# Performance work log

Measured on AMD Instinct MI355X. Metric: run time of the kernel, lower is better.

Reference implementation:

```python
import jax, jax.numpy as jnp
import numpy as np

B, C, H, W = 8, 384, 32, 32
N = 4                      # d_state
DI = 2 * C                 # d_inner = ssm_ratio * dim
R = -(-C // 16)            # dt_rank = ceil(dim/16) = 24
K = 4                      # scan directions
HID = 4 * C                # mlp hidden


def layer_norm(x, g, b, eps=1e-5):
    mu = jnp.mean(x, -1, keepdims=True)
    var = jnp.mean((x - mu) ** 2, -1, keepdims=True)
    return (x - mu) * jax.lax.rsqrt(var + eps) * g + b


def setup_inputs() -> dict:
    key = jax.random.key(0)
    ks = jax.random.split(key, 20)
    s = lambda k, shape, sc=0.02: jax.random.normal(k, shape, jnp.float32) * sc
    inp = {
        "x": jax.random.normal(ks[0], (B, C, H, W), jnp.float32),
        "ln1_g": jnp.ones((C,), jnp.float32), "ln1_b": jnp.zeros((C,), jnp.float32),
        "in_proj_W": s(ks[1], (2 * DI, C)),
        "conv_W": s(ks[2], (DI, 1, 3, 3), 0.1), "conv_b": jnp.zeros((DI,), jnp.float32),
        "x_proj_W": s(ks[3], (K, R + 2 * N, DI)),
        "dt_W": s(ks[4], (K, DI, R), 0.1), "dt_b": s(ks[5], (K, DI), 0.1),
        "A_log": jnp.log(jnp.tile(jnp.arange(1, N + 1, dtype=jnp.float32), (K, DI, 1))),
        "Ds": jnp.ones((K, DI), jnp.float32),
        "out_norm_g": jnp.ones((DI,), jnp.float32), "out_norm_b": jnp.zeros((DI,), jnp.float32),
        "out_proj_W": s(ks[6], (C, DI)),
        "ln2_g": jnp.ones((C,), jnp.float32), "ln2_b": jnp.zeros((C,), jnp.float32),
        "fc1_W": s(ks[7], (HID, C)), "fc1_b": jnp.zeros((HID,), jnp.float32),
        "fc2_W": s(ks[8], (C, HID)), "fc2_b": jnp.zeros((C,), jnp.float32),
    }
    return inp


def _block(x, ln1_g, ln1_b, in_proj_W, conv_W, conv_b, x_proj_W, dt_W, dt_b,
           A_log, Ds, out_norm_g, out_norm_b, out_proj_W, ln2_g, ln2_b,
           fc1_W, fc1_b, fc2_W, fc2_b):
    # x: (B,C,H,W) -> channels-last (B,H,W,C) as in mamba_fusion4
    xin = jnp.transpose(x, (0, 2, 3, 1))
    L = H * W
    shortcut = xin
    xn = layer_norm(xin, ln1_g, ln1_b)
    # ---- SS2D ----
    xz = jnp.einsum('bhwc,ec->bhwe', xn, in_proj_W)           # (B,H,W,2*DI)
    xs_, z = jnp.split(xz, 2, axis=-1)
    xc = jnp.transpose(xs_, (0, 3, 1, 2))                     # (B,DI,H,W)
    xc = jax.lax.conv_general_dilated(xc, conv_W, (1, 1), ((1, 1), (1, 1)),
                                      feature_group_count=DI)
    xc = jax.nn.silu(xc + conv_b[None, :, None, None])
    # cross-scan: 4 directions
    x_hw = xc.reshape(B, DI, L)
    x_wh = jnp.transpose(xc, (0, 1, 3, 2)).reshape(B, DI, L)
    xs = jnp.stack([x_hw, x_wh, jnp.flip(x_hw, -1), jnp.flip(x_wh, -1)], axis=1)  # (B,K,DI,L)
    x_dbl = jnp.einsum('bkdl,kcd->bkcl', xs, x_proj_W)
    dts, Bs, Cs = x_dbl[:, :, :R], x_dbl[:, :, R:R + N], x_dbl[:, :, R + N:]
    dts = jnp.einsum('bkrl,kdr->bkdl', dts, dt_W)
    dt = jax.nn.softplus(dts + dt_b[None, :, :, None])        # (B,K,DI,L)
    A = -jnp.exp(A_log)                                       # (K,DI,N)
    # selective scan, L-leading
    dt_l = jnp.transpose(dt, (3, 0, 1, 2))
    xs_l = jnp.transpose(xs, (3, 0, 1, 2))
    Bs_l = jnp.transpose(Bs, (3, 0, 1, 2))
    Cs_l = jnp.transpose(Cs, (3, 0, 1, 2))

    def step(h, inp):
        dtt, xt, Bt, Ct = inp                                  # (B,K,DI),(B,K,DI),(B,K,N),(B,K,N)
        h = jnp.exp(dtt[..., None] * A) * h + (dtt * xt)[..., None] * Bt[:, :, None, :]
        yt = jnp.einsum('bkdn,bkn->bkd', h, Ct)
        return h, yt

    h0 = jnp.zeros((B, K, DI, N), xs.dtype)
    _, ys = jax.lax.scan(step, h0, (dt_l, xs_l, Bs_l, Cs_l))   # ys: (L,B,K,DI)
    ys = jnp.transpose(ys, (1, 2, 3, 0))                       # (B,K,DI,L)
    ys = ys + xs * Ds[None, :, :, None]                        # skip D*u per direction
    # merge directions (invert flips / transposes)
    inv = jnp.flip(ys[:, 2:4], -1)
    wh = lambda t: jnp.transpose(t.reshape(B, DI, W, H), (0, 1, 3, 2)).reshape(B, DI, L)
    y = ys[:, 0] + inv[:, 0] + wh(ys[:, 1]) + wh(inv[:, 1])    # (B,DI,L)
    y = jnp.transpose(y, (0, 2, 1)).reshape(B, H, W, DI)
    y = layer_norm(y, out_norm_g, out_norm_b)
    y = y * jax.nn.silu(z)
    y = jnp.einsum('bhwd,cd->bhwc', y, out_proj_W)
    xr = shortcut + y
    # ---- MLP ----
    m = layer_norm(xr, ln2_g, ln2_b)
    m = jax.nn.gelu(jnp.einsum('bhwc,ec->bhwe', m, fc1_W) + fc1_b)
    m = jnp.einsum('bhwe,ce->bhwc', m, fc2_W) + fc2_b
    return xr + m                                              # (B,H,W,C)


def reference(x, ln1_g, ln1_b, in_proj_W, conv_W, conv_b, x_proj_W, dt_W, dt_b,
              A_log, Ds, out_norm_g, out_norm_b, out_proj_W, ln2_g, ln2_b,
              fc1_W, fc1_b, fc2_W, fc2_b):
    return _block(x, ln1_g, ln1_b, in_proj_W, conv_W, conv_b, x_proj_W, dt_W, dt_b,
                  A_log, Ds, out_norm_g, out_norm_b, out_proj_W, ln2_g, ln2_b,
                  fc1_W, fc1_b, fc2_W, fc2_b)
```

## Files before the change

### kernel.cpp

```cpp
#include <hip/hip_runtime.h>
#include <hip/hip_bf16.h>
#include <math.h>

#define LQ 1024
#define CC 384
#define DI 768
#define RR 24
#define NN 4
#define BB 8
#define NC 32
#define CL 32
#define LDP 40

typedef __attribute__((ext_vector_type(8))) short bf16x8;
typedef __attribute__((ext_vector_type(4))) float f32x4;

__device__ __forceinline__ float siluf(float v) { return v / (1.f + __expf(-v)); }
__device__ __forceinline__ float softplus_fast(float v) {
  float av = fabsf(v);
  float e = __expf(-av);
  return fmaxf(v, 0.f) + 0.69314718f * __log2f(1.f + e);
}
__device__ __forceinline__ float geluf(float x) {
  float u = 0.7978845608028654f * (x + 0.044715f * x * x * x);
  float e = __expf(2.f * u);
  float t = 1.f - 2.f / (e + 1.f);
  return 0.5f * x * (1.f + t);
}
__device__ __forceinline__ int trp(int l) { return ((l & 31) << 5) | (l >> 5); }
__device__ __forceinline__ short f2bf(float f) {
  union { float f; unsigned u; } v; v.f = f;
  unsigned r = (v.u + 0x7fffu + ((v.u >> 16) & 1u)) >> 16;
  return (short)r;
}
__device__ __forceinline__ float bf2f(unsigned short u) {
  union { unsigned u; float f; } v; v.u = ((unsigned)u) << 16; return v.f;
}
__device__ __forceinline__ bf16x8 pack8(float4 u, float4 v) {
  bf16x8 r;
  r[0] = f2bf(u.x); r[1] = f2bf(u.y); r[2] = f2bf(u.z); r[3] = f2bf(u.w);
  r[4] = f2bf(v.x); r[5] = f2bf(v.y); r[6] = f2bf(v.z); r[7] = f2bf(v.w);
  return r;
}
__device__ __forceinline__ void gload_lds16(const void* g, void* l) {
  __builtin_amdgcn_global_load_lds(
      (const __attribute__((address_space(1))) void*)g,
      (__attribute__((address_space(3))) void*)l, 16, 0, 0);
}
__device__ __forceinline__ void tile_barrier() {
  asm volatile("s_waitcnt lgkmcnt(0)" ::: "memory");
  __builtin_amdgcn_s_barrier();
  __builtin_amdgcn_sched_barrier(0);
}

__global__ __launch_bounds__(256) void wcvt_kernel(
    const float* __restrict__ w0, const float* __restrict__ w1,
    const float* __restrict__ w2, const float* __restrict__ w3,
    unsigned short* __restrict__ dst) {
  int gid = blockIdx.x * 256 + threadIdx.x;
  int e = gid * 8;
  const float* src; int off;
  if (e < 589824)        { src = w0; off = e; }
  else if (e < 884736)   { src = w1; off = e - 589824; }
  else if (e < 1474560)  { src = w2; off = e - 884736; }
  else                   { src = w3; off = e - 1474560; }
  float4 a = *(const float4*)(src + off);
  float4 b = *(const float4*)(src + off + 4);
  *(bf16x8*)(dst + e) = pack8(a, b);
}

__global__ __launch_bounds__(256) void ln1_transpose(
    const float* __restrict__ x, const float* __restrict__ g, const float* __restrict__ b,
    unsigned short* __restrict__ xn, unsigned short* __restrict__ xT) {
  __shared__ float xt[CC][65];
  __shared__ float reds[4][64], redq[4][64];
  __shared__ float mus[64], rvs[64];
  int blk = blockIdx.x;
  int bb = blk >> 4, l0 = (blk & 15) * 64;
  int tid = threadIdx.x;
  const float* xb = x + (size_t)bb * CC * LQ + l0;
#pragma unroll
  for (int it = 0; it < 96; ++it) {
// ... 207 lines not shown
  };
  auto storeT = [&](short* Ad, short* Wd, const uint4& pa, const float4* pw) {
    *(uint4*)&Ad[ar * LDP + ac] = pa;
    short* wdst = &Wd[wr * LDP + wc];
#pragma unroll
    for (int i = 0; i < WL / 2; ++i)
      *(bf16x8*)(wdst + i * 8) = pack8(pw[2 * i], pw[2 * i + 1]);
  };
  auto computeT = [&](const short* Ab, const short* Wb) {
    bf16x8 af[2], bf[NF];
#pragma unroll
    for (int i = 0; i < 2; ++i)
      af[i] = *(const bf16x8*)&Ab[(wm + i * 16 + l15) * LDP + l4 * 8];
#pragma unroll
    for (int j = 0; j < NF; ++j)
      bf[j] = *(const bf16x8*)&Wb[(wn + j * 16 + l15) * LDP + l4 * 8];
#pragma unroll
    for (int i = 0; i < 2; ++i)
#pragma unroll
      for (int j = 0; j < NF; ++j)
        acc[i][j] = __builtin_amdgcn_mfma_f32_16x16x32_bf16(af[i], bf[j], acc[i][j], 0, 0, 0);
  };

  const int NT = K >> 5;
  loadT(0, pa0, pw0);
  storeT(As0, Ws0, pa0, pw0);
  loadT(1, pa1, pw1);
  tile_barrier();
  for (int t = 0; t < NT; t += 2) {
    if (t + 2 < NT) loadT(t + 2, pa0, pw0);
    computeT(As0, Ws0);
    storeT(As1, Ws1, pa1, pw1);
    tile_barrier();
    if (t + 3 < NT) loadT(t + 3, pa1, pw1);
    computeT(As1, Ws1);
    if (t + 2 < NT) storeT(As0, Ws0, pa0, pw0);
    tile_barrier();
  }
#pragma unroll
  for (int i = 0; i < 2; ++i) {
    int mb = bm + wm + i * 16 + l4 * 4;
#pragma unroll
    for (int j = 0; j < NF; ++j) {
      int n = bn + wn + j * 16 + l15;
#pragma unroll
      for (int q = 0; q < 4; ++q) {
        int m = mb + q;
        ((float*)out0)[(size_t)m * N + n] = acc[i][j][q];
      }
    }
  }
}

__global__ __launch_bounds__(256) void dt_gemm(
    const float* __restrict__ xdbl, const float* __restrict__ dtW,
    const float* __restrict__ dtb, unsigned short* __restrict__ dt_all) {
  __shared__ short smem[128 * 136];
  short* As = smem;
  short* Ws = smem + 128 * LDP;
  const int tid = threadIdx.x;
  const int bm = blockIdx.x * 128;
  const int kk = blockIdx.y / 6, nt = blockIdx.y % 6;
  const int n0 = nt * 128;
  const int lane = tid & 63, w = tid >> 6;
  const int wm = (w >> 1) * 64, wn = (w & 1) * 64;
  const int l15 = lane & 15, l4 = lane >> 4;
  const int r = tid >> 1, half = (tid & 1) * 16;
  {
    const float* Ag = xdbl + (size_t)(bm + r) * 128 + kk * 32 + half;
    float4 a0 = *(const float4*)(Ag);
    float4 a1 = *(const float4*)(Ag + 4);
    float4 a2 = *(const float4*)(Ag + 8);
    float4 a3 = *(const float4*)(Ag + 12);
    short* asw = &As[r * LDP + half];
    *(bf16x8*)asw = pack8(a0, a1);
    *(bf16x8*)(asw + 8) = pack8(a2, a3);
    const float* Wg = dtW + ((size_t)kk * DI + n0 + r) * RR;
    bf16x8 qa, qb;
    if (half == 0) {
      float4 w0 = *(const float4*)(Wg);
      float4 w1 = *(const float4*)(Wg + 4);
      float4 w2 = *(const float4*)(Wg + 8);
      float4 w3 = *(const float4*)(Wg + 12);
      qa = pack8(w0, w1);
      qb = pack8(w2, w3);
    } else {
      float4 w0 = *(const float4*)(Wg + 16);
      float4 w1 = *(const float4*)(Wg + 20);
      qa = pack8(w0, w1);
      qb[0] = 0; qb[1] = 0; qb[2] = 0; qb[3] = 0;
      qb[4] = 0; qb[5] = 0; qb[6] = 0; qb[7] = 0;
    }
    short* wsw = &Ws[r * LDP + half];
    *(bf16x8*)wsw = qa;
    *(bf16x8*)(wsw + 8) = qb;
  }
  __syncthreads();
  f32x4 acc[4][4] = {};
  {
    const short* ap = &As[(wm + l15) * LDP + l4 * 8];
    const short* bp = &Ws[(wn + l15) * LDP + l4 * 8];
    bf16x8 af[4], bf[4];
#pragma unroll
    for (int f = 0; f < 4; ++f) af[f] = *(const bf16x8*)(ap + f * 16 * LDP);
#pragma unroll
    for (int f = 0; f < 4; ++f) bf[f] = *(const bf16x8*)(bp + f * 16 * LDP);
#pragma unroll
    for (int i = 0; i < 4; ++i)
#pragma unroll
      for (int j = 0; j < 4; ++j)
        acc[i][j] = __builtin_amdgcn_mfma_f32_16x16x32_bf16(af[i], bf[j], acc[i][j], 0, 0, 0);
  }
  __syncthreads();
#pragma unroll
  for (int j = 0; j < 4; ++j) {
    int col = wn + j * 16 + l15;
    float bv = dtb[kk * DI + n0 + col];
#pragma unroll
    for (int i = 0; i < 4; ++i) {
      int mrow = wm + i * 16 + l4 * 4;
#pragma unroll
      for (int q = 0; q < 4; ++q)
        smem[(mrow + q) * 136 + col] = f2bf(softplus_fast(acc[i][j][q] + bv));
    }
  }
  __syncthreads();
  const int row0 = tid >> 4, cg = (tid & 15) * 8;
#pragma unroll
  for (int it = 0; it < 8; ++it) {
    int row = row0 + it * 16;
    bf16x8 v = *(const bf16x8*)&smem[row * 136 + cg];
    *(bf16x8*)&dt_all[(size_t)(bm + row) * 3072 + kk * DI + n0 + cg] = v;
  }
}

__global__ __launch_bounds__(256) void conv_silu_kernel(
    const unsigned short* __restrict__ xs_, const float* __restrict__ cw,
    const float* __restrict__ cb, unsigned short* __restrict__ xcT) {
  int idx = blockIdx.x * 256 + threadIdx.x;
  int dg = idx % 96;
  int rem = idx / 96;
  int hq = rem & 7;
  int w = (rem >> 3) & 31;
  int b = rem >> 8;
  int d0 = dg * 8;
  int h0 = hq * 4;
  float wbuf[72];
#pragma unroll
  for (int i = 0; i < 18; ++i)
    *(float4*)&wbuf[i * 4] = *(const float4*)(cw + d0 * 9 + i * 4);
  float bias[8];
  *(float4*)&bias[0] = *(const float4*)(cb + d0);
  *(float4*)&bias[4] = *(const float4*)(cb + d0 + 4);
  float acc[4][8];
#pragma unroll
  for (int i = 0; i < 4; ++i)
#pragma unroll
    for (int j = 0; j < 8; ++j) acc[i][j] = bias[j];
  const unsigned short* xb = xs_ + (size_t)b * LQ * DI + d0;
#pragma unroll
  for (int hh = -1; hh <= 4; ++hh) {
    int h = h0 + hh;
    if (h < 0 || h > 31) continue;
#pragma unroll
    for (int dw = -1; dw <= 1; ++dw) {
      int ww = w + dw;
      if (ww < 0 || ww > 31) continue;
      bf16x8 xv = *(const bf16x8*)&xb[(size_t)(h * 32 + ww) * DI];
      float xf[8];
#pragma unroll
      for (int j = 0; j < 8; ++j) xf[j] = bf2f((unsigned short)xv[j]);
#pragma unroll
      for (int i = 0; i < 4; ++i) {
        int dh = hh - i;
        if (dh < -1 || dh > 1) continue;
        int tap = (dh + 1) * 3 + (dw + 1);
#pragma unroll
        for (int j = 0; j < 8; ++j) acc[i][j] += xf[j] * wbuf[j * 9 + tap];
      }
    }
  }
  unsigned short* ob = xcT + (size_t)b * LQ * DI + d0;
#pragma unroll
  for (int i = 0; i < 4; ++i) {
    bf16x8 v;
#pragma unroll
    for (int j = 0; j < 8; ++j) v[j] = f2bf(siluf(acc[i][j]));
    *(bf16x8*)&ob[(size_t)((h0 + i) * 32 + w) * DI] = v;
  }
}

__global__ __launch_bounds__(256) void scan_pass1(
    const unsigned short* __restrict__ xcT, const float* __restrict__ xdbl,
    const unsigned short* __restrict__ dtq,
    const float* __restrict__ A_log, float* __restrict__ Hc, float* __restrict__ Pc) {
  int c = blockIdx.x, dc = blockIdx.y, bk = blockIdx.z;
  int b = bk >> 2, k = bk & 3;
  int d = dc * 256 + threadIdx.x;
  float4 al = *(const float4*)&A_log[((size_t)k * DI + d) * NN];
  float A[NN] = {-__expf(al.x), -__expf(al.y), -__expf(al.z), -__expf(al.w)};
  float h[NN] = {0.f, 0.f, 0.f, 0.f}, P[NN] = {1.f, 1.f, 1.f, 1.f};
  const int kg = k & 1;
  const bool fl = k >= 2;
  int pos0 = kg ? c : c * CL;
  int dpos = kg ? 32 : 1;
  if (fl) { pos0 = 1023 - pos0; dpos = -dpos; }
  const unsigned short* dtp = dtq + ((size_t)b * LQ + pos0) * 3072 + k * DI + d;
  const unsigned short* xcp = xcT + ((size_t)b * LQ + pos0) * DI + d;
  const float* xdp = xdbl + ((size_t)b * LQ + pos0) * 128 + k * 32 + 24;
  const ptrdiff_t sDT = (ptrdiff_t)dpos * 3072;
  const ptrdiff_t sXC = (ptrdiff_t)dpos * DI;
  const ptrdiff_t sXD = (ptrdiff_t)dpos * 128;
  for (int j = 0; j < CL; ++j) {
    float dt = bf2f(*dtp);
    float xv = bf2f(*xcp);
    float4 Bv = *(const float4*)xdp;
    float dx = dt * xv;
    float a;
    a = __expf(dt * A[0]); h[0] = a * h[0] + dx * Bv.x; P[0] *= a;
    a = __expf(dt * A[1]); h[1] = a * h[1] + dx * Bv.y; P[1] *= a;
    a = __expf(dt * A[2]); h[2] = a * h[2] + dx * Bv.z; P[2] *= a;
    a = __expf(dt * A[3]); h[3] = a * h[3] + dx * Bv.w; P[3] *= a;
    dtp += sDT; xcp += sXC; xdp += sXD;
  }
  size_t base = (((size_t)bk * NC + c) * DI + d) * 4;
  *(float4*)&Hc[base] = make_float4(h[0], h[1], h[2], h[3]);
  *(float4*)&Pc[base] = make_float4(P[0], P[1], P[2], P[3]);
}

__global__ __launch_bounds__(256) void scan_pass2(
    float* __restrict__ Hc, const float* __restrict__ Pc) {
  int idx = blockIdx.x * 256 + threadIdx.x;
  int bk = idx / DI, d = idx - bk * DI;
  float4 hin = make_float4(0.f, 0.f, 0.f, 0.f);
  for (int c = 0; c < NC; ++c) {
    size_t base = (((size_t)bk * NC + c) * DI + d) * 4;
    float4 hl = *(const float4*)&Hc[base];
    float4 p = *(const float4*)&Pc[base];
    *(float4*)&Hc[base] = hin;
    hin.x = hl.x + p.x * hin.x;
    hin.y = hl.y + p.y * hin.y;
    hin.z = hl.z + p.z * hin.z;
    hin.w = hl.w + p.w * hin.w;
  }
}

__global__ __launch_bounds__(256) void scan_pass3(
    const unsigned short* __restrict__ xcT, const float* __restrict__ xdbl,
    const unsigned short* __restrict__ dtq,
    const float* __restrict__ A_log, const float* __restrict__ Ds,
    const float* __restrict__ Hin,
    unsigned short* __restrict__ ym1, unsigned short* __restrict__ ym2) {
  __shared__ unsigned short ylds[CL][256];
  int c = blockIdx.x, dc = blockIdx.y, bg = blockIdx.z;
  int b = bg >> 1, g = bg & 1;
  int tid = threadIdx.x;
  int d = dc * 256 + tid;
  int ka = g, kb = g + 2;
  int ca = c, cb = NC - 1 - c;
  float4 ala = *(const float4*)&A_log[((size_t)ka * DI + d) * NN];
  float4 alb = *(const float4*)&A_log[((size_t)kb * DI + d) * NN];
  float Aa[NN] = {-__expf(ala.x), -__expf(ala.y), -__expf(ala.z), -__expf(ala.w)};
  float Ab[NN] = {-__expf(alb.x), -__expf(alb.y), -__expf(alb.z), -__expf(alb.w)};
  float Da = Ds[ka * DI + d], Db = Ds[kb * DI + d];
  size_t basea = (((size_t)(b * 4 + ka) * NC + ca) * DI + d) * 4;
  size_t baseb = (((size_t)(b * 4 + kb) * NC + cb) * DI + d) * 4;
  float4 h4a = *(const float4*)&Hin[basea];
  float4 h4b = *(const float4*)&Hin[baseb];
  float ha[NN] = {h4a.x, h4a.y, h4a.z, h4a.w};
  float hb[NN] = {h4b.x, h4b.y, h4b.z, h4b.w};
  unsigned short* ym = g ? ym2 : ym1;
  int pa0 = g ? ca : ca * CL;
  int dpa = g ? 32 : 1;
  int pb0 = g ? (1023 - cb) : (1023 - cb * CL);
  const unsigned short* dta_p = dtq + ((size_t)b * LQ + pa0) * 3072 + ka * DI + d;
  const unsigned short* dtb_p = dtq + ((size_t)b * LQ + pb0) * 3072 + kb * DI + d;
  const unsigned short* xca_p = xcT + ((size_t)b * LQ + pa0) * DI + d;
  const unsigned short* xcb_p = xcT + ((size_t)b * LQ + pb0) * DI + d;
  const float* xda_p = xdbl + ((size_t)b * LQ + pa0) * 128 + ka * 32 + 24;
  const float* xdb_p = xdbl + ((size_t)b * LQ + pb0) * 128 + kb * 32 + 24;
  const ptrdiff_t sDT = (ptrdiff_t)dpa * 3072;
  const ptrdiff_t sXC = (ptrdiff_t)dpa * DI;
  const ptrdiff_t sXD = (ptrdiff_t)dpa * 128;
  for (int j = 0; j < CL; ++j) {
    float dta = bf2f(*dta_p);
    float dtb2 = bf2f(*dtb_p);
    float xa = bf2f(*xca_p);
    float xb = bf2f(*xcb_p);
    float4 Ba = *(const float4*)xda_p;
    float4 Ca = *(const float4*)(xda_p + 4);
    float4 Bb = *(const float4*)xdb_p;
    float4 Cb = *(const float4*)(xdb_p + 4);
    float dxa = dta * xa, dxb = dtb2 * xb;
    float ya = xa * Da, yb = xb * Db;
    float a;
    a = __expf(dta * Aa[0]); ha[0] = a * ha[0] + dxa * Ba.x; ya += ha[0] * Ca.x;
    a = __expf(dta * Aa[1]); ha[1] = a * ha[1] + dxa * Ba.y; ya += ha[1] * Ca.y;
    a = __expf(dta * Aa[2]); ha[2] = a * ha[2] + dxa * Ba.z; ya += ha[2] * Ca.z;
    a = __expf(dta * Aa[3]); ha[3] = a * ha[3] + dxa * Ba.w; ya += ha[3] * Ca.w;
    a = __expf(dtb2 * Ab[0]); hb[0] = a * hb[0] + dxb * Bb.x; yb += hb[0] * Cb.x;
    a = __expf(dtb2 * Ab[1]); hb[1] = a * hb[1] + dxb * Bb.y; yb += hb[1] * Cb.y;
    a = __expf(dtb2 * Ab[2]); hb[2] = a * hb[2] + dxb * Bb.z; yb += hb[2] * Cb.z;
    a = __expf(dtb2 * Ab[3]); hb[3] = a * hb[3] + dxb * Bb.w; yb += hb[3] * Cb.w;
    if (j < CL / 2) {
      ylds[j][tid] = (unsigned short)f2bf(ya);
      ylds[CL - 1 - j][tid] = (unsigned short)f2bf(yb);
    } else {
      ylds[j][tid] = (unsigned short)f2bf(bf2f(ylds[j][tid]) + ya);
      ylds[CL - 1 - j][tid] = (unsigned short)f2bf(bf2f(ylds[CL - 1 - j][tid]) + yb);
    }
    dta_p += sDT; dtb_p -= sDT;
    xca_p += sXC; xcb_p -= sXC;
    xda_p += sXD; xdb_p -= sXD;
  }
  unsigned short* ymp = ym + ((size_t)b * LQ + pa0) * DI + d;
  for (int s = 0; s < CL; ++s) {
    *ymp = ylds[s][tid];
    ymp += sXC;
  }
}

__global__ __launch_bounds__(256) void outnorm_mult_kernel(
    const unsigned short* __restrict__ ym1, const unsigned short* __restrict__ ym2,
    const unsigned short* __restrict__ z, const float* __restrict__ g,
    const float* __restrict__ bta, unsigned short* __restrict__ out) {
  int t = blockIdx.x, tid = threadIdx.x;
  __shared__ float red[8];
  float v[3]; float s = 0.f, sq = 0.f;
#pragma unroll
  for (int i = 0; i < 3; ++i) {
    int dd = tid + i * 256;
    float y = bf2f(ym1[(size_t)t * DI + dd]) + bf2f(ym2[(size_t)t * DI + dd]);
    v[i] = y; s += y; sq += y * y;
  }
#pragma unroll
  for (int off = 32; off > 0; off >>= 1) { s += __shfl_xor(s, off); sq += __shfl_xor(sq, off); }
  int wid = tid >> 6;
  if ((tid & 63) == 0) { red[wid] = s; red[4 + wid] = sq; }
  __syncthreads();
  s = red[0] + red[1] + red[2] + red[3];
  sq = red[4] + red[5] + red[6] + red[7];
  float mu = s * (1.f / DI), var = sq * (1.f / DI) - mu * mu;
  float r = rsqrtf(var + 1e-5f);
#pragma unroll
  for (int i = 0; i < 3; ++i) {
    int dd = tid + i * 256;
    float zv = bf2f(z[(size_t)t * DI + dd]);
    out[(size_t)t * DI + dd] =
        (unsigned short)f2bf(((v[i] - mu) * r * g[dd] + bta[dd]) * siluf(zv));
  }
}

extern "C" void kernel_launch(void* const* d_in, const int* in_sizes, int n_in,
                              void* d_out, int out_size, void* d_ws, size_t ws_size,
                              hipStream_t stream) {
  const float* x          = (const float*)d_in[0];
  const float* ln1_g      = (const float*)d_in[1];
  const float* ln1_b      = (const float*)d_in[2];
  const float* in_proj_W  = (const float*)d_in[3];
  const float* conv_W     = (const float*)d_in[4];
  const float* conv_b     = (const float*)d_in[5];
  const float* x_proj_W   = (const float*)d_in[6];
  const float* dt_W       = (const float*)d_in[7];
  const float* dt_b       = (const float*)d_in[8];
  const float* A_log      = (const float*)d_in[9];
  const float* Ds         = (const float*)d_in[10];
  const float* out_norm_g = (const float*)d_in[11];
  const float* out_norm_b = (const float*)d_in[12];
  const float* out_proj_W = (const float*)d_in[13];
  const float* ln2_g      = (const float*)d_in[14];
  const float* ln2_b      = (const float*)d_in[15];
  const float* fc1_W      = (const float*)d_in[16];
  const float* fc1_b      = (const float*)d_in[17];
  const float* fc2_W      = (const float*)d_in[18];
  const float* fc2_b      = (const float*)d_in[19];

  const int M = BB * LQ;
  char* RA = (char*)d_ws;
  char* RB = RA + 12582912;
  char* RC = RB + 25165824;
  char* RD = RC + 12582912;
  char* RE = RD + 25165824;
  char* RF = RE + 12582912;
  char* RG = RF + 4194304;
  char* RH = RG + 50331648;

  unsigned short* xn  = (unsigned short*)RA;
  float*          Hc  = (float*)RA;
  float*          xr  = (float*)RA;
  unsigned short* xs_ = (unsigned short*)RB;
  float*          Pc  = (float*)RB;
  unsigned short* ym1 = (unsigned short*)RB;
  unsigned short* m1  = (unsigned short*)RB;
  unsigned short* z   = (unsigned short*)RC;
  unsigned short* m0  = (unsigned short*)RC;
  unsigned short* ym2 = (unsigned short*)RD;
  unsigned short* xcT = (unsigned short*)RE;
  unsigned short* mn  = (unsigned short*)RE;
  float*          xdbl = (float*)RF;
  unsigned short* dtq = (unsigned short*)RG;
  unsigned short* xT  = (unsigned short*)RH;
  unsigned short* wbf = (unsigned short*)(RH + 6291456);
  unsigned short* wb_inproj  = wbf;
  unsigned short* wb_outproj = wbf + 589824;
  unsigned short* wb_fc1     = wbf + 884736;
  unsigned short* wb_fc2     = wbf + 1474560;

  wcvt_kernel<<<1008, 256, 0, stream>>>(in_proj_W, out_proj_W, fc1_W, fc2_W, wbf);
  ln1_transpose<<<128, 256, 0, stream>>>(x, ln1_g, ln1_b, xn, xT);
  gemm_lds<0, 128><<<dim3(M / 128, 12), 256, 0, stream>>>(
      xn, wb_inproj, xs_, z, nullptr, nullptr, M, 1536, CC);
  conv_silu_kernel<<<768, 256, 0, stream>>>(xs_, conv_W, conv_b, xcT);
  gemm_mfma<4, 64><<<dim3(M / 64, 2), 256, 0, stream>>>(
      xcT, x_proj_W, xdbl, nullptr, nullptr, nullptr, M, 128, DI);
  dt_gemm<<<dim3(M / 128, 24), 256, 0, stream>>>(xdbl, dt_W, dt_b, dtq);
  scan_pass1<<<dim3(NC, 3, BB * 4), 256, 0, stream>>>(
      xcT, xdbl, dtq, A_log, Hc, Pc);
  scan_pass2<<<(BB * 4 * DI) / 256, 256, 0, stream>>>(Hc, Pc);
  scan_pass3<<<dim3(NC, 3, BB * 2), 256, 0, stream>>>(
      xcT, xdbl, dtq, A_log, Ds, Hc, ym1, ym2);
  outnorm_mult_kernel<<<M, 256, 0, stream>>>(ym1, ym2, z, out_norm_g, out_norm_b, mn);
  gemm_lds<1, 64><<<dim3(M / 64, 3), 256, 0, stream>>>(
      mn, wb_outproj, xr, nullptr, nullptr, xT, M, 384, DI);
  ln2_kernel<<<M, 64, 0, stream>>>(xr, ln2_g, ln2_b, m0);
  gemm_lds<2, 128><<<dim3(M / 128, 12), 256, 0, stream>>>(
      m0, wb_fc1, m1, nullptr, fc1_b, nullptr, M, 1536, CC);
  gemm_lds<3, 64><<<dim3(M / 64, 3), 256, 0, stream>>>(
      m1, wb_fc2, (float*)d_out, nullptr, fc2_b, xr, M, 384, 1536);
}
```

Baseline: 227.7 us.

## Fuse dt projection and softplus into scan passes, drop dt_gemm

New measurement: 282.6 us. +24.1%, slower.

```diff
diff --git a/kernel.cpp b/kernel.cpp
--- a/kernel.cpp
+++ b/kernel.cpp
@@ -341,88 +341,6 @@
   }
 }
 
-__global__ __launch_bounds__(256) void dt_gemm(
-    const float* __restrict__ xdbl, const float* __restrict__ dtW,
-    const float* __restrict__ dtb, unsigned short* __restrict__ dt_all) {
-  __shared__ short smem[128 * 136];
-  short* As = smem;
-  short* Ws = smem + 128 * LDP;
-  const int tid = threadIdx.x;
-  const int bm = blockIdx.x * 128;
-  const int kk = blockIdx.y / 6, nt = blockIdx.y % 6;
-  const int n0 = nt * 128;
-  const int lane = tid & 63, w = tid >> 6;
-  const int wm = (w >> 1) * 64, wn = (w & 1) * 64;
-  const int l15 = lane & 15, l4 = lane >> 4;
-  const int r = tid >> 1, half = (tid & 1) * 16;
-  {
-    const float* Ag = xdbl + (size_t)(bm + r) * 128 + kk * 32 + half;
-    float4 a0 = *(const float4*)(Ag);
-    float4 a1 = *(const float4*)(Ag + 4);
-    float4 a2 = *(const float4*)(Ag + 8);
-    float4 a3 = *(const float4*)(Ag + 12);
-    short* asw = &As[r * LDP + half];
-    *(bf16x8*)asw = pack8(a0, a1);
-    *(bf16x8*)(asw + 8) = pack8(a2, a3);
-    const float* Wg = dtW + ((size_t)kk * DI + n0 + r) * RR;
-    bf16x8 qa, qb;
-    if (half == 0) {
-      float4 w0 = *(const float4*)(Wg);
-      float4 w1 = *(const float4*)(Wg + 4);
-      float4 w2 = *(const float4*)(Wg + 8);
-      float4 w3 = *(const float4*)(Wg + 12);
-      qa = pack8(w0, w1);
-      qb = pack8(w2, w3);
-    } else {
-      float4 w0 = *(const float4*)(Wg + 16);
-      float4 w1 = *(const float4*)(Wg + 20);
-      qa = pack8(w0, w1);
-      qb[0] = 0; qb[1] = 0; qb[2] = 0; qb[3] = 0;
-      qb[4] = 0; qb[5] = 0; qb[6] = 0; qb[7] = 0;
-    }
-    short* wsw = &Ws[r * LDP + half];
-    *(bf16x8*)wsw = qa;
-    *(bf16x8*)(wsw + 8) = qb;
-  }
-  __syncthreads();
-  f32x4 acc[4][4] = {};
-  {
-    const short* ap = &As[(wm + l15) * LDP + l4 * 8];
-    const short* bp = &Ws[(wn + l15) * LDP + l4 * 8];
-    bf16x8 af[4], bf[4];
-#pragma unroll
-    for (int f = 0; f < 4; ++f) af[f] = *(const bf16x8*)(ap + f * 16 * LDP);
-#pragma unroll
-    for (int f = 0; f < 4; ++f) bf[f] = *(const bf16x8*)(bp + f * 16 * LDP);
-#pragma unroll
-    for (int i = 0; i < 4; ++i)
-#pragma unroll
-      for (int j = 0; j < 4; ++j)
-        acc[i][j] = __builtin_amdgcn_mfma_f32_16x16x32_bf16(af[i], bf[j], acc[i][j], 0, 0, 0);
-  }
-  __syncthreads();
-#pragma unroll
-  for (int j = 0; j < 4; ++j) {
-    int col = wn + j * 16 + l15;
-    float bv = dtb[kk * DI + n0 + col];
-#pragma unroll
-    for (int i = 0; i < 4; ++i) {
-      int mrow = wm + i * 16 + l4 * 4;
-#pragma unroll
-      for (int q = 0; q < 4; ++q)
-        smem[(mrow + q) * 136 + col] = f2bf(softplus_fast(acc[i][j][q] + bv));
-    }
-  }
-  __syncthreads();
-  const int row0 = tid >> 4, cg = (tid & 15) * 8;
-#pragma unroll
-  for (int it = 0; it < 8; ++it) {
-    int row = row0 + it * 16;
-    bf16x8 v = *(const bf16x8*)&smem[row * 136 + cg];
-    *(bf16x8*)&dt_all[(size_t)(bm + row) * 3072 + kk * DI + n0 + cg] = v;
-  }
-}
-
 __global__ __launch_bounds__(256) void conv_silu_kernel(
     const unsigned short* __restrict__ xs_, const float* __restrict__ cw,
     const float* __restrict__ cb, unsigned short* __restrict__ xcT) {
@@ -481,36 +399,51 @@
 
 __global__ __launch_bounds__(256) void scan_pass1(
     const unsigned short* __restrict__ xcT, const float* __restrict__ xdbl,
-    const unsigned short* __restrict__ dtq,
+    const float* __restrict__ dtW, const float* __restrict__ dtb,
     const float* __restrict__ A_log, float* __restrict__ Hc, float* __restrict__ Pc) {
+  __shared__ float xl[CL][36];
   int c = blockIdx.x, dc = blockIdx.y, bk = blockIdx.z;
   int b = bk >> 2, k = bk & 3;
-  int d = dc * 256 + threadIdx.x;
-  float4 al = *(const float4*)&A_log[((size_t)k * DI + d) * NN];
-  float A[NN] = {-__expf(al.x), -__expf(al.y), -__expf(al.z), -__expf(al.w)};
-  float h[NN] = {0.f, 0.f, 0.f, 0.f}, P[NN] = {1.f, 1.f, 1.f, 1.f};
+  int tid = threadIdx.x;
+  int d = dc * 256 + tid;
   const int kg = k & 1;
   const bool fl = k >= 2;
   int pos0 = kg ? c : c * CL;
   int dpos = kg ? 32 : 1;
   if (fl) { pos0 = 1023 - pos0; dpos = -dpos; }
-  const unsigned short* dtp = dtq + ((size_t)b * LQ + pos0) * 3072 + k * DI + d;
+  {
+    int j = tid >> 3, q = tid & 7;
+    int pos = pos0 + j * dpos;
+    *(float4*)&xl[j][q * 4] =
+        *(const float4*)(xdbl + ((size_t)b * LQ + pos) * 128 + k * 32 + q * 4);
+  }
+  float4 al = *(const float4*)&A_log[((size_t)k * DI + d) * NN];
+  float A[NN] = {-__expf(al.x), -__expf(al.y), -__expf(al.z), -__expf(al.w)};
+  float w[RR];
+  const float* wp = dtW + ((size_t)k * DI + d) * RR;
+#pragma unroll
+  for (int r = 0; r < RR; r += 4) {
+    float4 t4 = *(const float4*)(wp + r);
+    w[r] = t4.x; w[r + 1] = t4.y; w[r + 2] = t4.z; w[r + 3] = t4.w;
+  }
+  float dbias = dtb[k * DI + d];
+  float h[NN] = {0.f, 0.f, 0.f, 0.f}, P[NN] = {1.f, 1.f, 1.f, 1.f};
   const unsigned short* xcp = xcT + ((size_t)b * LQ + pos0) * DI + d;
-  const float* xdp = xdbl + ((size_t)b * LQ + pos0) * 128 + k * 32 + 24;
-  const ptrdiff_t sDT = (ptrdiff_t)dpos * 3072;
   const ptrdiff_t sXC = (ptrdiff_t)dpos * DI;
-  const ptrdiff_t sXD = (ptrdiff_t)dpos * 128;
+  __syncthreads();
   for (int j = 0; j < CL; ++j) {
-    float dt = bf2f(*dtp);
+    float dtr = dbias;
+#pragma unroll
+    for (int r = 0; r < RR; ++r) dtr += xl[j][r] * w[r];
+    float dt = softplus_fast(dtr);
     float xv = bf2f(*xcp);
-    float4 Bv = *(const float4*)xdp;
     float dx = dt * xv;
     float a;
-    a = __expf(dt * A[0]); h[0] = a * h[0] + dx * Bv.x; P[0] *= a;
-    a = __expf(dt * A[1]); h[1] = a * h[1] + dx * Bv.y; P[1] *= a;
-    a = __expf(dt * A[2]); h[2] = a * h[2] + dx * Bv.z; P[2] *= a;
-    a = __expf(dt * A[3]); h[3] = a * h[3] + dx * Bv.w; P[3] *= a;
-    dtp += sDT; xcp += sXC; xdp += sXD;
+    a = __expf(dt * A[0]); h[0] = a * h[0] + dx * xl[j][24]; P[0] *= a;
+    a = __expf(dt * A[1]); h[1] = a * h[1] + dx * xl[j][25]; P[1] *= a;
+    a = __expf(dt * A[2]); h[2] = a * h[2] + dx * xl[j][26]; P[2] *= a;
+    a = __expf(dt * A[3]); h[3] = a * h[3] + dx * xl[j][27]; P[3] *= a;
+    xcp += sXC;
   }
   size_t base = (((size_t)bk * NC + c) * DI + d) * 4;
   *(float4*)&Hc[base] = make_float4(h[0], h[1], h[2], h[3]);
@@ -536,22 +469,46 @@
 
 __global__ __launch_bounds__(256) void scan_pass3(
     const unsigned short* __restrict__ xcT, const float* __restrict__ xdbl,
-    const unsigned short* __restrict__ dtq,
+    const float* __restrict__ dtW, const float* __restrict__ dtb,
     const float* __restrict__ A_log, const float* __restrict__ Ds,
     const float* __restrict__ Hin,
     unsigned short* __restrict__ ym1, unsigned short* __restrict__ ym2) {
   __shared__ unsigned short ylds[CL][256];
+  __shared__ float xla[CL][36], xlb[CL][36];
   int c = blockIdx.x, dc = blockIdx.y, bg = blockIdx.z;
   int b = bg >> 1, g = bg & 1;
   int tid = threadIdx.x;
   int d = dc * 256 + tid;
   int ka = g, kb = g + 2;
   int ca = c, cb = NC - 1 - c;
+  int pa0 = g ? ca : ca * CL;
+  int dpa = g ? 32 : 1;
+  int pb0 = g ? (1023 - cb) : (1023 - cb * CL);
+  {
+    int j = tid >> 3, q = tid & 7;
+    int posa = pa0 + j * dpa;
+    int posb = pb0 - j * dpa;
+    *(float4*)&xla[j][q * 4] =
+        *(const float4*)(xdbl + ((size_t)b * LQ + posa) * 128 + ka * 32 + q * 4);
+    *(float4*)&xlb[j][q * 4] =
+        *(const float4*)(xdbl + ((size_t)b * LQ + posb) * 128 + kb * 32 + q * 4);
+  }
   float4 ala = *(const float4*)&A_log[((size_t)ka * DI + d) * NN];
   float4 alb = *(const float4*)&A_log[((size_t)kb * DI + d) * NN];
   float Aa[NN] = {-__expf(ala.x), -__expf(ala.y), -__expf(ala.z), -__expf(ala.w)};
   float Ab[NN] = {-__expf(alb.x), -__expf(alb.y), -__expf(alb.z), -__expf(alb.w)};
   float Da = Ds[ka * DI + d], Db = Ds[kb * DI + d];
+  float wa[RR], wb[RR];
+  const float* wap = dtW + ((size_t)ka * DI + d) * RR;
+  const float* wbp = dtW + ((size_t)kb * DI + d) * RR;
+#pragma unroll
+  for (int r = 0; r < RR; r += 4) {
+    float4 t4 = *(const float4*)(wap + r);
+    wa[r] = t4.x; wa[r + 1] = t4.y; wa[r + 2] = t4.z; wa[r + 3] = t4.w;
+    float4 u4 = *(const float4*)(wbp + r);
+    wb[r] = u4.x; wb[r + 1] = u4.y; wb[r + 2] = u4.z; wb[r + 3] = u4.w;
+  }
+  float biasa = dtb[ka * DI + d], biasb = dtb[kb * DI + d];
   size_t basea = (((size_t)(b * 4 + ka) * NC + ca) * DI + d) * 4;
   size_t baseb = (((size_t)(b * 4 + kb) * NC + cb) * DI + d) * 4;
   float4 h4a = *(const float4*)&Hin[basea];
@@ -559,38 +516,32 @@
   float ha[NN] = {h4a.x, h4a.y, h4a.z, h4a.w};
   float hb[NN] = {h4b.x, h4b.y, h4b.z, h4b.w};
   unsigned short* ym = g ? ym2 : ym1;
-  int pa0 = g ? ca : ca * CL;
-  int dpa = g ? 32 : 1;
-  int pb0 = g ? (1023 - cb) : (1023 - cb * CL);
-  const unsigned short* dta_p = dtq + ((size_t)b * LQ + pa0) * 3072 + ka * DI + d;
-  const unsigned short* dtb_p = dtq + ((size_t)b * LQ + pb0) * 3072 + kb * DI + d;
   const unsigned short* xca_p = xcT + ((size_t)b * LQ + pa0) * DI + d;
   const unsigned short* xcb_p = xcT + ((size_t)b * LQ + pb0) * DI + d;
-  const float* xda_p = xdbl + ((size_t)b * LQ + pa0) * 128 + ka * 32 + 24;
-  const float* xdb_p = xdbl + ((size_t)b * LQ + pb0) * 128 + kb * 32 + 24;
-  const ptrdiff_t sDT = (ptrdiff_t)dpa * 3072;
   const ptrdiff_t sXC = (ptrdiff_t)dpa * DI;
-  const ptrdiff_t sXD = (ptrdiff_t)dpa * 128;
+  __syncthreads();
   for (int j = 0; j < CL; ++j) {
-    float dta = bf2f(*dta_p);
-    float dtb2 = bf2f(*dtb_p);
+    float dtra = biasa, dtrb = biasb;
+#pragma unroll
+    for (int r = 0; r < RR; ++r) {
+      dtra += xla[j][r] * wa[r];
+      dtrb += xlb[j][r] * wb[r];
+    }
+    float dta = softplus_fast(dtra);
+    float dtb2 = softplus_fast(dtrb);
     float xa = bf2f(*xca_p);
     float xb = bf2f(*xcb_p);
-    float4 Ba = *(const float4*)xda_p;
-    float4 Ca = *(const float4*)(xda_p + 4);
-    float4 Bb = *(const float4*)xdb_p;
-    float4 Cb = *(const float4*)(xdb_p + 4);
     float dxa = dta * xa, dxb = dtb2 * xb;
     float ya = xa * Da, yb = xb * Db;
     float a;
-    a = __expf(dta * Aa[0]); ha[0] = a * ha[0] + dxa * Ba.x; ya += ha[0] * Ca.x;
-    a = __expf(dta * Aa[1]); ha[1] = a * ha[1] + dxa * Ba.y; ya += ha[1] * Ca.y;
-    a = __expf(dta * Aa[2]); ha[2] = a * ha[2] + dxa * Ba.z; ya += ha[2] * Ca.z;
-    a = __expf(dta * Aa[3]); ha[3] = a * ha[3] + dxa * Ba.w; ya += ha[3] * Ca.w;
-    a = __expf(dtb2 * Ab[0]); hb[0] = a * hb[0] + dxb * Bb.x; yb += hb[0] * Cb.x;
-    a = __expf(dtb2 * Ab[1]); hb[1] = a * hb[1] + dxb * Bb.y; yb += hb[1] * Cb.y;
-    a = __expf(dtb2 * Ab[2]); hb[2] = a * hb[2] + dxb * Bb.z; yb += hb[2] * Cb.z;
-    a = __expf(dtb2 * Ab[3]); hb[3] = a * hb[3] + dxb * Bb.w; yb += hb[3] * Cb.w;
+    a = __expf(dta * Aa[0]); ha[0] = a * ha[0] + dxa * xla[j][24]; ya += ha[0] * xla[j][28];
+    a = __expf(dta * Aa[1]); ha[1] = a * ha[1] + dxa * xla[j][25]; ya += ha[1] * xla[j][29];
+    a = __expf(dta * Aa[2]); ha[2] = a * ha[2] + dxa * xla[j][26]; ya += ha[2] * xla[j][30];
+    a = __expf(dta * Aa[3]); ha[3] = a * ha[3] + dxa * xla[j][27]; ya += ha[3] * xla[j][31];
+    a = __expf(dtb2 * Ab[0]); hb[0] = a * hb[0] + dxb * xlb[j][24]; yb += hb[0] * xlb[j][28];
+    a = __expf(dtb2 * Ab[1]); hb[1] = a * hb[1] + dxb * xlb[j][25]; yb += hb[1] * xlb[j][29];
+    a = __expf(dtb2 * Ab[2]); hb[2] = a * hb[2] + dxb * xlb[j][26]; yb += hb[2] * xlb[j][30];
+    a = __expf(dtb2 * Ab[3]); hb[3] = a * hb[3] + dxb * xlb[j][27]; yb += hb[3] * xlb[j][31];
     if (j < CL / 2) {
       ylds[j][tid] = (unsigned short)f2bf(ya);
       ylds[CL - 1 - j][tid] = (unsigned short)f2bf(yb);
@@ -598,9 +549,7 @@
       ylds[j][tid] = (unsigned short)f2bf(bf2f(ylds[j][tid]) + ya);
       ylds[CL - 1 - j][tid] = (unsigned short)f2bf(bf2f(ylds[CL - 1 - j][tid]) + yb);
     }
-    dta_p += sDT; dtb_p -= sDT;
     xca_p += sXC; xcb_p -= sXC;
-    xda_p += sXD; xdb_p -= sXD;
   }
   unsigned short* ymp = ym + ((size_t)b * LQ + pa0) * DI + d;
   for (int s = 0; s < CL; ++s) {
@@ -687,7 +636,6 @@
   unsigned short* xcT = (unsigned short*)RE;
   unsigned short* mn  = (unsigned short*)RE;
   float*          xdbl = (float*)RF;
-  unsigned short* dtq = (unsigned short*)RG;
   unsigned short* xT  = (unsigned short*)RH;
   unsigned short* wbf = (unsigned short*)(RH + 6291456);
   unsigned short* wb_inproj  = wbf;
@@ -702,12 +650,11 @@
   conv_silu_kernel<<<768, 256, 0, stream>>>(xs_, conv_W, conv_b, xcT);
   gemm_mfma<4, 64><<<dim3(M / 64, 2), 256, 0, stream>>>(
       xcT, x_proj_W, xdbl, nullptr, nullptr, nullptr, M, 128, DI);
-  dt_gemm<<<dim3(M / 128, 24), 256, 0, stream>>>(xdbl, dt_W, dt_b, dtq);
   scan_pass1<<<dim3(NC, 3, BB * 4), 256, 0, stream>>>(
-      xcT, xdbl, dtq, A_log, Hc, Pc);
+      xcT, xdbl, dt_W, dt_b, A_log, Hc, Pc);
   scan_pass2<<<(BB * 4 * DI) / 256, 256, 0, stream>>>(Hc, Pc);
   scan_pass3<<<dim3(NC, 3, BB * 2), 256, 0, stream>>>(
-      xcT, xdbl, dtq, A_log, Ds, Hc, ym1, ym2);
+      xcT, xdbl, dt_W, dt_b, A_log, Ds, Hc, ym1, ym2);
   outnorm_mult_kernel<<<M, 256, 0, stream>>>(ym1, ym2, z, out_norm_g, out_norm_b, mn);
   gemm_lds<1, 64><<<dim3(M / 64, 3), 256, 0, stream>>>(
       mn, wb_outproj, xr, nullptr, nullptr, xT, M, 384, DI);
```

## Prefetch scan inputs, stage B/C in LDS, compute chunk decay from dt sum

Applied to the files above, without the earlier changes.

Result: slower. 246.8 us (+8.4%).

```diff
diff --git a/kernel.cpp b/kernel.cpp
--- a/kernel.cpp
+++ b/kernel.cpp
@@ -483,54 +483,89 @@
     const unsigned short* __restrict__ xcT, const float* __restrict__ xdbl,
     const unsigned short* __restrict__ dtq,
     const float* __restrict__ A_log, float* __restrict__ Hc, float* __restrict__ Pc) {
+  __shared__ float xlB[CL][4];
   int c = blockIdx.x, dc = blockIdx.y, bk = blockIdx.z;
   int b = bk >> 2, k = bk & 3;
-  int d = dc * 256 + threadIdx.x;
-  float4 al = *(const float4*)&A_log[((size_t)k * DI + d) * NN];
-  float A[NN] = {-__expf(al.x), -__expf(al.y), -__expf(al.z), -__expf(al.w)};
-  float h[NN] = {0.f, 0.f, 0.f, 0.f}, P[NN] = {1.f, 1.f, 1.f, 1.f};
+  int tid = threadIdx.x;
+  int d = dc * 256 + tid;
   const int kg = k & 1;
   const bool fl = k >= 2;
   int pos0 = kg ? c : c * CL;
   int dpos = kg ? 32 : 1;
   if (fl) { pos0 = 1023 - pos0; dpos = -dpos; }
+  if (tid < CL) {
+    int pos = pos0 + tid * dpos;
+    *(float4*)&xlB[tid][0] =
+        *(const float4*)(xdbl + ((size_t)b * LQ + pos) * 128 + k * 32 + 24);
+  }
+  float4 al = *(const float4*)&A_log[((size_t)k * DI + d) * NN];
+  float A[NN] = {-__expf(al.x), -__expf(al.y), -__expf(al.z), -__expf(al.w)};
+  float h[NN] = {0.f, 0.f, 0.f, 0.f};
+  float sdt = 0.f;
   const unsigned short* dtp = dtq + ((size_t)b * LQ + pos0) * 3072 + k * DI + d;
   const unsigned short* xcp = xcT + ((size_t)b * LQ + pos0) * DI + d;
-  const float* xdp = xdbl + ((size_t)b * LQ + pos0) * 128 + k * 32 + 24;
   const ptrdiff_t sDT = (ptrdiff_t)dpos * 3072;
   const ptrdiff_t sXC = (ptrdiff_t)dpos * DI;
-  const ptrdiff_t sXD = (ptrdiff_t)dpos * 128;
-  for (int j = 0; j < CL; ++j) {
-    float dt = bf2f(*dtp);
-    float xv = bf2f(*xcp);
-    float4 Bv = *(const float4*)xdp;
-    float dx = dt * xv;
-    float a;
-    a = __expf(dt * A[0]); h[0] = a * h[0] + dx * Bv.x; P[0] *= a;
-    a = __expf(dt * A[1]); h[1] = a * h[1] + dx * Bv.y; P[1] *= a;
-    a = __expf(dt * A[2]); h[2] = a * h[2] + dx * Bv.z; P[2] *= a;
-    a = __expf(dt * A[3]); h[3] = a * h[3] + dx * Bv.w; P[3] *= a;
-    dtp += sDT; xcp += sXC; xdp += sXD;
+  float dv[2][4], xv[2][4];
+#pragma unroll
+  for (int u = 0; u < 4; ++u) {
+    dv[0][u] = bf2f(dtp[(ptrdiff_t)u * sDT]);
+    xv[0][u] = bf2f(xcp[(ptrdiff_t)u * sXC]);
+  }
+  __syncthreads();
+#pragma unroll
+  for (int gg = 0; gg < 8; ++gg) {
+    const int cur = gg & 1, nxt = cur ^ 1;
+    if (gg < 7) {
+#pragma unroll
+      for (int u = 0; u < 4; ++u) {
+        int j = (gg + 1) * 4 + u;
+        dv[nxt][u] = bf2f(dtp[(ptrdiff_t)j * sDT]);
+        xv[nxt][u] = bf2f(xcp[(ptrdiff_t)j * sXC]);
+      }
+    }
+#pragma unroll
+    for (int u = 0; u < 4; ++u) {
+      int j = gg * 4 + u;
+      float dt = dv[cur][u], xval = xv[cur][u];
+      float4 Bv = *(const float4*)&xlB[j][0];
+      float dx = dt * xval;
+      sdt += dt;
+      float a;
+      a = __expf(dt * A[0]); h[0] = a * h[0] + dx * Bv.x;
+      a = __expf(dt * A[1]); h[1] = a * h[1] + dx * Bv.y;
+      a = __expf(dt * A[2]); h[2] = a * h[2] + dx * Bv.z;
+      a = __expf(dt * A[3]); h[3] = a * h[3] + dx * Bv.w;
+    }
   }
   size_t base = (((size_t)bk * NC + c) * DI + d) * 4;
   *(float4*)&Hc[base] = make_float4(h[0], h[1], h[2], h[3]);
-  *(float4*)&Pc[base] = make_float4(P[0], P[1], P[2], P[3]);
+  *(float4*)&Pc[base] = make_float4(__expf(sdt * A[0]), __expf(sdt * A[1]),
+                                    __expf(sdt * A[2]), __expf(sdt * A[3]));
 }
 
 __global__ __launch_bounds__(256) void scan_pass2(
     float* __restrict__ Hc, const float* __restrict__ Pc) {
   int idx = blockIdx.x * 256 + threadIdx.x;
   int bk = idx / DI, d = idx - bk * DI;
+  size_t base0 = (((size_t)bk * NC) * DI + d) * 4;
+  const size_t cstr = (size_t)DI * 4;
   float4 hin = make_float4(0.f, 0.f, 0.f, 0.f);
+  float4 hl = *(const float4*)&Hc[base0];
+  float4 p  = *(const float4*)&Pc[base0];
   for (int c = 0; c < NC; ++c) {
-    size_t base = (((size_t)bk * NC + c) * DI + d) * 4;
-    float4 hl = *(const float4*)&Hc[base];
-    float4 p = *(const float4*)&Pc[base];
-    *(float4*)&Hc[base] = hin;
+    float4 hl_n = hl, p_n = p;
+    if (c + 1 < NC) {
+      size_t bn = base0 + (size_t)(c + 1) * cstr;
+      hl_n = *(const float4*)&Hc[bn];
+      p_n  = *(const float4*)&Pc[bn];
+    }
+    *(float4*)&Hc[base0 + (size_t)c * cstr] = hin;
     hin.x = hl.x + p.x * hin.x;
     hin.y = hl.y + p.y * hin.y;
     hin.z = hl.z + p.z * hin.z;
     hin.w = hl.w + p.w * hin.w;
+    hl = hl_n; p = p_n;
   }
 }
 
@@ -541,12 +576,28 @@
     const float* __restrict__ Hin,
     unsigned short* __restrict__ ym1, unsigned short* __restrict__ ym2) {
   __shared__ unsigned short ylds[CL][256];
+  __shared__ float xbca[CL][8], xbcb[CL][8];
   int c = blockIdx.x, dc = blockIdx.y, bg = blockIdx.z;
   int b = bg >> 1, g = bg & 1;
   int tid = threadIdx.x;
   int d = dc * 256 + tid;
   int ka = g, kb = g + 2;
   int ca = c, cb = NC - 1 - c;
+  int pa0 = g ? ca : ca * CL;
+  int dpa = g ? 32 : 1;
+  int pb0 = g ? (1023 - cb) : (1023 - cb * CL);
+  if (tid < CL) {
+    int pos = pa0 + tid * dpa;
+    const float* p = xdbl + ((size_t)b * LQ + pos) * 128 + ka * 32 + 24;
+    *(float4*)&xbca[tid][0] = *(const float4*)p;
+    *(float4*)&xbca[tid][4] = *(const float4*)(p + 4);
+  } else if (tid < 2 * CL) {
+    int t2 = tid - CL;
+    int pos = pb0 - t2 * dpa;
+    const float* p = xdbl + ((size_t)b * LQ + pos) * 128 + kb * 32 + 24;
+    *(float4*)&xbcb[t2][0] = *(const float4*)p;
+    *(float4*)&xbcb[t2][4] = *(const float4*)(p + 4);
+  }
   float4 ala = *(const float4*)&A_log[((size_t)ka * DI + d) * NN];
   float4 alb = *(const float4*)&A_log[((size_t)kb * DI + d) * NN];
   float Aa[NN] = {-__expf(ala.x), -__expf(ala.y), -__expf(ala.z), -__expf(ala.w)};
@@ -559,48 +610,62 @@
   float ha[NN] = {h4a.x, h4a.y, h4a.z, h4a.w};
   float hb[NN] = {h4b.x, h4b.y, h4b.z, h4b.w};
   unsigned short* ym = g ? ym2 : ym1;
-  int pa0 = g ? ca : ca * CL;
-  int dpa = g ? 32 : 1;
-  int pb0 = g ? (1023 - cb) : (1023 - cb * CL);
   const unsigned short* dta_p = dtq + ((size_t)b * LQ + pa0) * 3072 + ka * DI + d;
   const unsigned short* dtb_p = dtq + ((size_t)b * LQ + pb0) * 3072 + kb * DI + d;
   const unsigned short* xca_p = xcT + ((size_t)b * LQ + pa0) * DI + d;
   const unsigned short* xcb_p = xcT + ((size_t)b * LQ + pb0) * DI + d;
-  const float* xda_p = xdbl + ((size_t)b * LQ + pa0) * 128 + ka * 32 + 24;
-  const float* xdb_p = xdbl + ((size_t)b * LQ + pb0) * 128 + kb * 32 + 24;
   const ptrdiff_t sDT = (ptrdiff_t)dpa * 3072;
   const ptrdiff_t sXC = (ptrdiff_t)dpa * DI;
-  const ptrdiff_t sXD = (ptrdiff_t)dpa * 128;
-  for (int j = 0; j < CL; ++j) {
-    float dta = bf2f(*dta_p);
-    float dtb2 = bf2f(*dtb_p);
-    float xa = bf2f(*xca_p);
-    float xb = bf2f(*xcb_p);
-    float4 Ba = *(const float4*)xda_p;
-    float4 Ca = *(const float4*)(xda_p + 4);
-    float4 Bb = *(const float4*)xdb_p;
-    float4 Cb = *(const float4*)(xdb_p + 4);
-    float dxa = dta * xa, dxb = dtb2 * xb;
-    float ya = xa * Da, yb = xb * Db;
-    float a;
-    a = __expf(dta * Aa[0]); ha[0] = a * ha[0] + dxa * Ba.x; ya += ha[0] * Ca.x;
-    a = __expf(dta * Aa[1]); ha[1] = a * ha[1] + dxa * Ba.y; ya += ha[1] * Ca.y;
-    a = __expf(dta * Aa[2]); ha[2] = a * ha[2] + dxa * Ba.z; ya += ha[2] * Ca.z;
-    a = __expf(dta * Aa[3]); ha[3] = a * ha[3] + dxa * Ba.w; ya += ha[3] * Ca.w;
-    a = __expf(dtb2 * Ab[0]); hb[0] = a * hb[0] + dxb * Bb.x; yb += hb[0] * Cb.x;
-    a = __expf(dtb2 * Ab[1]); hb[1] = a * hb[1] + dxb * Bb.y; yb += hb[1] * Cb.y;
-    a = __expf(dtb2 * Ab[2]); hb[2] = a * hb[2] + dxb * Bb.z; yb += hb[2] * Cb.z;
-    a = __expf(dtb2 * Ab[3]); hb[3] = a * hb[3] + dxb * Bb.w; yb += hb[3] * Cb.w;
-    if (j < CL / 2) {
-      ylds[j][tid] = (unsigned short)f2bf(ya);
-      ylds[CL - 1 - j][tid] = (unsigned short)f2bf(yb);
-    } else {
-      ylds[j][tid] = (unsigned short)f2bf(bf2f(ylds[j][tid]) + ya);
-      ylds[CL - 1 - j][tid] = (unsigned short)f2bf(bf2f(ylds[CL - 1 - j][tid]) + yb);
-    }
-    dta_p += sDT; dtb_p -= sDT;
-    xca_p += sXC; xcb_p -= sXC;
-    xda_p += sXD; xdb_p -= sXD;
+  float dva[2][4], dvb[2][4], xva[2][4], xvb[2][4];
+#pragma unroll
+  for (int u = 0; u < 4; ++u) {
+    dva[0][u] = bf2f(dta_p[(ptrdiff_t)u * sDT]);
+    dvb[0][u] = bf2f(dtb_p[-(ptrdiff_t)u * sDT]);
+    xva[0][u] = bf2f(xca_p[(ptrdiff_t)u * sXC]);
+    xvb[0][u] = bf2f(xcb_p[-(ptrdiff_t)u * sXC]);
+  }
+  __syncthreads();
+#pragma unroll
+  for (int gg = 0; gg < 8; ++gg) {
+    const int cur = gg & 1, nxt = cur ^ 1;
+    if (gg < 7) {
+#pragma unroll
+      for (int u = 0; u < 4; ++u) {
+        int j = (gg + 1) * 4 + u;
+        dva[nxt][u] = bf2f(dta_p[(ptrdiff_t)j * sDT]);
+        dvb[nxt][u] = bf2f(dtb_p[-(ptrdiff_t)j * sDT]);
+        xva[nxt][u] = bf2f(xca_p[(ptrdiff_t)j * sXC]);
+        xvb[nxt][u] = bf2f(xcb_p[-(ptrdiff_t)j * sXC]);
+      }
+    }
+#pragma unroll
+    for (int u = 0; u < 4; ++u) {
+      int j = gg * 4 + u;
+      float dta = dva[cur][u], dtb2 = dvb[cur][u];
+      float xa = xva[cur][u], xb = xvb[cur][u];
+      float4 Ba = *(const float4*)&xbca[j][0];
+      float4 Ca = *(const float4*)&xbca[j][4];
+      float4 Bb = *(const float4*)&xbcb[j][0];
+      float4 Cb = *(const float4*)&xbcb[j][4];
+      float dxa = dta * xa, dxb = dtb2 * xb;
+      float ya = xa * Da, yb = xb * Db;
+      float a;
+      a = __expf(dta * Aa[0]); ha[0] = a * ha[0] + dxa * Ba.x; ya += ha[0] * Ca.x;
+      a = __expf(dta * Aa[1]); ha[1] = a * ha[1] + dxa * Ba.y; ya += ha[1] * Ca.y;
+      a = __expf(dta * Aa[2]); ha[2] = a * ha[2] + dxa * Ba.z; ya += ha[2] * Ca.z;
+      a = __expf(dta * Aa[3]); ha[3] = a * ha[3] + dxa * Ba.w; ya += ha[3] * Ca.w;
+      a = __expf(dtb2 * Ab[0]); hb[0] = a * hb[0] + dxb * Bb.x; yb += hb[0] * Cb.x;
+      a = __expf(dtb2 * Ab[1]); hb[1] = a * hb[1] + dxb * Bb.y; yb += hb[1] * Cb.y;
+      a = __expf(dtb2 * Ab[2]); hb[2] = a * hb[2] + dxb * Bb.z; yb += hb[2] * Cb.z;
+      a = __expf(dtb2 * Ab[3]); hb[3] = a * hb[3] + dxb * Bb.w; yb += hb[3] * Cb.w;
+      if (j < CL / 2) {
+        ylds[j][tid] = (unsigned short)f2bf(ya);
+        ylds[CL - 1 - j][tid] = (unsigned short)f2bf(yb);
+      } else {
+        ylds[j][tid] = (unsigned short)f2bf(bf2f(ylds[j][tid]) + ya);
+        ylds[CL - 1 - j][tid] = (unsigned short)f2bf(bf2f(ylds[CL - 1 - j][tid]) + yb);
+      }
+    }
   }
   unsigned short* ymp = ym + ((size_t)b * LQ + pa0) * DI + d;
   for (int s = 0; s < CL; ++s) {
```

## Parallelize chunk-carry scan with warp shuffles and compute decay from summed dt

Applied to the files above, without the earlier changes.

After: 230.1 us. Within noise of the previous version (+1.0%).

```diff
diff --git a/kernel.cpp b/kernel.cpp
--- a/kernel.cpp
+++ b/kernel.cpp
@@ -27,7 +27,6 @@
   float t = 1.f - 2.f / (e + 1.f);
   return 0.5f * x * (1.f + t);
 }
-__device__ __forceinline__ int trp(int l) { return ((l & 31) << 5) | (l >> 5); }
 __device__ __forceinline__ short f2bf(float f) {
   union { float f; unsigned u; } v; v.f = f;
   unsigned r = (v.u + 0x7fffu + ((v.u >> 16) & 1u)) >> 16;
@@ -488,7 +487,8 @@
   int d = dc * 256 + threadIdx.x;
   float4 al = *(const float4*)&A_log[((size_t)k * DI + d) * NN];
   float A[NN] = {-__expf(al.x), -__expf(al.y), -__expf(al.z), -__expf(al.w)};
-  float h[NN] = {0.f, 0.f, 0.f, 0.f}, P[NN] = {1.f, 1.f, 1.f, 1.f};
+  float h[NN] = {0.f, 0.f, 0.f, 0.f};
+  float sdt = 0.f;
   const int kg = k & 1;
   const bool fl = k >= 2;
   int pos0 = kg ? c : c * CL;
@@ -505,33 +505,45 @@
     float xv = bf2f(*xcp);
     float4 Bv = *(const float4*)xdp;
     float dx = dt * xv;
+    sdt += dt;
     float a;
-    a = __expf(dt * A[0]); h[0] = a * h[0] + dx * Bv.x; P[0] *= a;
-    a = __expf(dt * A[1]); h[1] = a * h[1] + dx * Bv.y; P[1] *= a;
-    a = __expf(dt * A[2]); h[2] = a * h[2] + dx * Bv.z; P[2] *= a;
-    a = __expf(dt * A[3]); h[3] = a * h[3] + dx * Bv.w; P[3] *= a;
+    a = __expf(dt * A[0]); h[0] = a * h[0] + dx * Bv.x;
+    a = __expf(dt * A[1]); h[1] = a * h[1] + dx * Bv.y;
+    a = __expf(dt * A[2]); h[2] = a * h[2] + dx * Bv.z;
+    a = __expf(dt * A[3]); h[3] = a * h[3] + dx * Bv.w;
     dtp += sDT; xcp += sXC; xdp += sXD;
   }
   size_t base = (((size_t)bk * NC + c) * DI + d) * 4;
   *(float4*)&Hc[base] = make_float4(h[0], h[1], h[2], h[3]);
-  *(float4*)&Pc[base] = make_float4(P[0], P[1], P[2], P[3]);
+  *(float4*)&Pc[base] = make_float4(__expf(sdt * A[0]), __expf(sdt * A[1]),
+                                    __expf(sdt * A[2]), __expf(sdt * A[3]));
 }
 
 __global__ __launch_bounds__(256) void scan_pass2(
     float* __restrict__ Hc, const float* __restrict__ Pc) {
-  int idx = blockIdx.x * 256 + threadIdx.x;
-  int bk = idx / DI, d = idx - bk * DI;
-  float4 hin = make_float4(0.f, 0.f, 0.f, 0.f);
-  for (int c = 0; c < NC; ++c) {
-    size_t base = (((size_t)bk * NC + c) * DI + d) * 4;
-    float4 hl = *(const float4*)&Hc[base];
-    float4 p = *(const float4*)&Pc[base];
-    *(float4*)&Hc[base] = hin;
-    hin.x = hl.x + p.x * hin.x;
-    hin.y = hl.y + p.y * hin.y;
-    hin.z = hl.z + p.z * hin.z;
-    hin.w = hl.w + p.w * hin.w;
-  }
+  int t = blockIdx.x * 256 + threadIdx.x;
+  int c = t & 31;
+  int chain = t >> 5;
+  int bk = chain / DI, d = chain - bk * DI;
+  size_t base = (((size_t)bk * NC + c) * DI + d) * 4;
+  float4 h = *(const float4*)&Hc[base];
+  float4 p = *(const float4*)&Pc[base];
+#pragma unroll
+  for (int s = 1; s < NC; s <<= 1) {
+    float hx = __shfl_up(h.x, s, 32), hy = __shfl_up(h.y, s, 32);
+    float hz = __shfl_up(h.z, s, 32), hw = __shfl_up(h.w, s, 32);
+    float px = __shfl_up(p.x, s, 32), py = __shfl_up(p.y, s, 32);
+    float pz = __shfl_up(p.z, s, 32), pw = __shfl_up(p.w, s, 32);
+    if (c >= s) {
+      h.x += p.x * hx; h.y += p.y * hy; h.z += p.z * hz; h.w += p.w * hw;
+      p.x *= px; p.y *= py; p.z *= pz; p.w *= pw;
+    }
+  }
+  float4 he;
+  he.x = __shfl_up(h.x, 1, 32); he.y = __shfl_up(h.y, 1, 32);
+  he.z = __shfl_up(h.z, 1, 32); he.w = __shfl_up(h.w, 1, 32);
+  if (c == 0) { he.x = 0.f; he.y = 0.f; he.z = 0.f; he.w = 0.f; }
+  *(float4*)&Hc[base] = he;
 }
 
 __global__ __launch_bounds__(256) void scan_pass3(
@@ -705,7 +717,7 @@
   dt_gemm<<<dim3(M / 128, 24), 256, 0, stream>>>(xdbl, dt_W, dt_b, dtq);
   scan_pass1<<<dim3(NC, 3, BB * 4), 256, 0, stream>>>(
       xcT, xdbl, dtq, A_log, Hc, Pc);
-  scan_pass2<<<(BB * 4 * DI) / 256, 256, 0, stream>>>(Hc, Pc);
+  scan_pass2<<<3072, 256, 0, stream>>>(Hc, Pc);
   scan_pass3<<<dim3(NC, 3, BB * 2), 256, 0, stream>>>(
       xcT, xdbl, dtq, A_log, Ds, Hc, ym1, ym2);
   outnorm_mult_kernel<<<M, 256, 0, stream>>>(ym1, ym2, z, out_norm_g, out_norm_b, mn);
```
